# Kernel optimization log

Measured on AMD Instinct MI355X. Metric: run time of the kernel, lower is better.

The kernel has to match this reference:

```python
import jax, jax.numpy as jnp
import numpy as np

B, C, H, W = 64, 64, 56, 56
MID = 2 * C  # two output nodes concatenated
EPS = 1e-5


def _conv1x1(x, w):
    # x: [B,C,H,W], w: [O,C] (1x1 conv kernel squeezed)
    return jnp.einsum('bchw,oc->bohw', x, w)


def _bn(x, g, b, m, v):
    # eval-mode BatchNorm2d with running stats
    sc = g * jax.lax.rsqrt(v + EPS)
    return x * sc[None, :, None, None] + (b - m * sc)[None, :, None, None]


def _maxpool3(x):
    # MaxPool2d(kernel=3, stride=1, padding=1)
    return jax.lax.reduce_window(x, -jnp.inf, jax.lax.max,
                                 (1, 1, 3, 3), (1, 1, 1, 1),
                                 [(0, 0), (0, 0), (1, 1), (1, 1)])


def _avgpool3(x):
    # AvgPool2d(kernel=3, stride=1, padding=1), count_include_pad=True -> /9
    s = jax.lax.reduce_window(x, 0.0, jax.lax.add,
                              (1, 1, 3, 3), (1, 1, 1, 1),
                              [(0, 0), (0, 0), (1, 1), (1, 1)])
    return s * (1.0 / 9.0)


def setup_inputs() -> dict:
    key = jax.random.key(0)
    ks = jax.random.split(key, 11)
    x = jax.random.normal(ks[0], (B, C, H, W), dtype=jnp.float32)
    w1 = jax.random.normal(ks[1], (C, C), dtype=jnp.float32) * 0.1
    w2 = jax.random.normal(ks[2], (C, MID), dtype=jnp.float32) * 0.1
    bn1_g = 1.0 + 0.1 * jax.random.normal(ks[3], (C,), dtype=jnp.float32)
    bn1_b = 0.1 * jax.random.normal(ks[4], (C,), dtype=jnp.float32)
    bn1_m = 0.1 * jax.random.normal(ks[5], (C,), dtype=jnp.float32)
    bn1_v = jax.random.uniform(ks[6], (C,), minval=0.5, maxval=1.5, dtype=jnp.float32)
    bn2_g = 1.0 + 0.1 * jax.random.normal(ks[7], (C,), dtype=jnp.float32)
    bn2_b = 0.1 * jax.random.normal(ks[8], (C,), dtype=jnp.float32)
    bn2_m = 0.1 * jax.random.normal(ks[9], (C,), dtype=jnp.float32)
    bn2_v = jax.random.uniform(ks[10], (C,), minval=0.5, maxval=1.5, dtype=jnp.float32)
    return dict(x=x, w1=w1, w2=w2,
                bn1_g=bn1_g, bn1_b=bn1_b, bn1_m=bn1_m, bn1_v=bn1_v,
                bn2_g=bn2_g, bn2_b=bn2_b, bn2_m=bn2_m, bn2_v=bn2_v)


def reference(x, w1, w2, bn1_g, bn1_b, bn1_m, bn1_v, bn2_g, bn2_b, bn2_m, bn2_v):
    # DAG g = [[[0,1],[1,2]], [[4,3],[3]], [[5,3],[3,100]], [[4,3],[100]]]
    # topoSort order: [0, 2, 1, 3]; output nodes (ordered): [2, 3]
    node0 = jax.nn.relu(_bn(_conv1x1(x, w1), bn1_g, bn1_b, bn1_m, bn1_v))
    node1 = _maxpool3(node0)            # op type 4, pred {0}
    node2 = _avgpool3(node0)            # op type 5, pred {0}
    node3 = _maxpool3(node1) + _maxpool3(node2)  # op type 4, preds {1,2}, summed
    cat = jnp.concatenate([node2, node3], axis=1)  # [B, 2C, H, W]
    out = jax.nn.relu(_bn(_conv1x1(cat, w2), bn2_g, bn2_b, bn2_m, bn2_v))
    return out
```

## Files before the change

### kernel.cpp

```cpp
#include <hip/hip_runtime.h>
#include <cstddef>

#define EPS 1e-5f
static constexpr int Bn = 64, Cn = 64, Hn = 56, Wn = 56, HWn = Hn * Wn;
static constexpr int RB = 14;
static constexpr int NBAND = 4;
static constexpr int PR = 5;
static constexpr int SLAB5 = 2256;

typedef __attribute__((ext_vector_type(8))) short short8;
typedef __attribute__((ext_vector_type(4))) unsigned short ushort4v;
typedef __attribute__((ext_vector_type(4))) float floatx4;
typedef __attribute__((ext_vector_type(16))) float floatx16;
typedef __attribute__((ext_vector_type(4))) unsigned int uintx4;
typedef __attribute__((ext_vector_type(2))) unsigned int uintx2;

__device__ __forceinline__ unsigned pack_rne(float a, float b) {
    unsigned ua = __float_as_uint(a), ub = __float_as_uint(b);
    ua = ua + 0x7fffu + ((ua >> 16) & 1u);
    ub = ub + 0x7fffu + ((ub >> 16) & 1u);
    return __builtin_amdgcn_perm(ub, ua, 0x07060302);
}
__device__ __forceinline__ unsigned pack_trunc(float a, float b) {
    return __builtin_amdgcn_perm(__float_as_uint(b), __float_as_uint(a), 0x07060302);
}
__device__ __forceinline__ uintx2 pmax2(uintx2 a, uintx2 b) {
    ushort4v r = __builtin_elementwise_max(*(ushort4v*)&a, *(ushort4v*)&b);
    return *(uintx2*)&r;
}
__device__ __forceinline__ float bf_lo(unsigned u) { return __uint_as_float(u << 16); }
__device__ __forceinline__ float bf_hi(unsigned u) { return __uint_as_float(u & 0xffff0000u); }


__global__ __launch_bounds__(256, 3) void k1_conv1(
    const float* __restrict__ x, const float* __restrict__ w1,
    const float* __restrict__ bg, const float* __restrict__ bb,
    const float* __restrict__ bm, const float* __restrict__ bv,
    unsigned short* __restrict__ node0)
{
    __shared__ float scs[64], shs[64];
    const int tid = threadIdx.x;
    if (tid < 64) {
        float sc = bg[tid] * rsqrtf(bv[tid] + EPS);
        scs[tid] = sc;
        shs[tid] = bb[tid] - bm[tid] * sc;
    }
    __syncthreads();
    const int lane = tid & 63;
    const int wv   = tid >> 6;
    const int n    = lane & 31;
    const int h    = lane >> 5;

    short8 afr0[4], afr1[4];
    {
        const float s0 = scs[n], s1 = scs[32 + n];
        #pragma unroll
        for (int kt = 0; kt < 4; ++kt) {
            const float* wp0 = w1 + (size_t)n * 64 + kt * 16 + h * 8;
            floatx4 f0 = *(const floatx4*)wp0;
            floatx4 f1 = *(const floatx4*)(wp0 + 4);
            uintx4 u;
            u.x = pack_rne(f0[0] * s0, f0[1] * s0);
            u.y = pack_rne(f0[2] * s0, f0[3] * s0);
            u.z = pack_rne(f1[0] * s0, f1[1] * s0);
            u.w = pack_rne(f1[2] * s0, f1[3] * s0);
            afr0[kt] = *(short8*)&u;
            const float* wp1 = wp0 + 32 * 64;
            floatx4 g0 = *(const floatx4*)wp1;
            floatx4 g1 = *(const floatx4*)(wp1 + 4);
            uintx4 v;
            v.x = pack_rne(g0[0] * s1, g0[1] * s1);
            v.y = pack_rne(g0[2] * s1, g0[3] * s1);
            v.z = pack_rne(g1[0] * s1, g1[1] * s1);
            v.w = pack_rne(g1[2] * s1, g1[3] * s1);
            afr1[kt] = *(short8*)&v;
        }
    }

    const int bid = blockIdx.x;
    const int xcd = bid & 7;
    const int idx = bid >> 3;
    const int P = (xcd * 98 + idx) * 256 + wv * 64;
    const int b = P / HWn, p0 = P - b * HWn;
    const float* xb = x + (size_t)b * 64 * HWn + p0 + n;

    float f0[4][8], f1[4][8];
    #pragma unroll
    for (int kt = 0; kt < 4; ++kt)
        #pragma unroll
        for (int j = 0; j < 8; ++j) {
            const float* xp = xb + (size_t)(kt * 16 + h * 8 + j) * HWn;
            f0[kt][j] = xp[0];
            f1[kt][j] = xp[32];
        }

    #pragma unroll
    for (int s = 0; s < 2; ++s) {
        floatx16 acc0, acc1;
        #pragma unroll
        for (int i = 0; i < 16; ++i) { acc0[i] = 0.f; acc1[i] = 0.f; }

        #pragma unroll
        for (int kt = 0; kt < 4; ++kt) {
            float* fr = s ? f1[kt] : f0[kt];
            uintx4 u;
            u.x = pack_trunc(fr[0], fr[1]);
            u.y = pack_trunc(fr[2], fr[3]);
            u.z = pack_trunc(fr[4], fr[5]);
            u.w = pack_trunc(fr[6], fr[7]);
            short8 bfr = *(short8*)&u;
            acc0 = __builtin_amdgcn_mfma_f32_32x32x16_bf16(afr0[kt], bfr, acc0, 0, 0, 0);
            acc1 = __builtin_amdgcn_mfma_f32_32x32x16_bf16(afr1[kt], bfr, acc1, 0, 0, 0);
        }

        #pragma unroll
        for (int oct = 0; oct < 2; ++oct) {
            #pragma unroll
            for (int g = 0; g < 4; ++g) {
                floatx4 sh4 = *(const floatx4*)&shs[oct * 32 + g * 8 + h * 4];
                float v0 = (oct ? acc1[g * 4 + 0] : acc0[g * 4 + 0]) + sh4[0]; v0 = v0 > 0.f ? v0 : 0.f;
                float v1 = (oct ? acc1[g * 4 + 1] : acc0[g * 4 + 1]) + sh4[1]; v1 = v1 > 0.f ? v1 : 0.f;
                float v2 = (oct ? acc1[g * 4 + 2] : acc0[g * 4 + 2]) + sh4[2]; v2 = v2 > 0.f ? v2 : 0.f;
                float v3 = (oct ? acc1[g * 4 + 3] : acc0[g * 4 + 3]) + sh4[3]; v3 = v3 > 0.f ? v3 : 0.f;
                uintx2 st;
                st.x = pack_rne(v0, v1);
                st.y = pack_rne(v2, v3);
                const int chunk = oct * 4 + g;
                *(uintx2*)(node0 + ((size_t)(b * 8 + chunk) * HWn + p0 + s * 32 + n) * 8 + h * 4) = st;
            }
        }
    }
}

__global__ __launch_bounds__(1024, 1) void k23_fused(
    const unsigned short* __restrict__ node0,
    const float* __restrict__ w2,
    const float* __restrict__ bg, const float* __restrict__ bb,
    const float* __restrict__ bm, const float* __restrict__ bv,
    float* __restrict__ out)
{
    __shared__ __align__(16) unsigned short catl[2 * 16 * SLAB5 + 64];
    const int tid = threadIdx.x;
    const int lane = tid & 63;
    const int wv = tid >> 6;

    const int bid = blockIdx.x;
    const int xcd = bid & 7;
    const int jj = bid >> 3;
    const int b = xcd * 8 + (jj >> 2);
    const int band = jj & 3;
    const int lo = band * RB;

    const int chunk = wv >> 1;
    const int c0 = (wv & 1) * 28;
    const int local = lane >> 1;
    const int col = c0 - 2 + local;
    const int jh = lane & 1;
    const bool stcol = (local >= 2) & (local <= 29);
    const unsigned short* nbase = node0 + ((size_t)(b * 8 + chunk) * HWn) * 8 + jh * 4;

    const int m16 = lane & 15;
    const int q = lane >> 4;
    const int t = wv & 3;
    const int e = wv >> 2;
    short8 afr[4];
    #pragma unroll
    for (int cp = 0; cp < 4; ++cp) {
        const int c = 2 * cp + (q >> 1);
        const int chb = ((q & 1) ? 64 : 0) + 8 * c;
        const float* wp = w2 + (size_t)(t * 16 + m16) * 128 + chb;
        floatx4 f0 = *(const floatx4*)wp;
        floatx4 f1 = *(const floatx4*)(wp + 4);
        uintx4 u;
        u.x = pack_rne(f0[0], f0[1]);
        u.y = pack_rne(f0[2], f0[3]);
        u.z = pack_rne(f1[0], f1[1]);
        u.w = pack_rne(f1[2], f1[3]);
        afr[cp] = *(short8*)&u;
    }
    const int oc0 = t * 16 + q * 4;
    floatx4 g4 = *(const floatx4*)(bg + oc0);
    floatx4 bb4 = *(const floatx4*)(bb + oc0);
    floatx4 mm4 = *(const floatx4*)(bm + oc0);
    floatx4 vv4 = *(const floatx4*)(bv + oc0);
    float sc2[4], sh2[4];
    #pragma unroll
    for (int r = 0; r < 4; ++r) {
        sc2[r] = g4[r] * rsqrtf(vv4[r] + EPS);
        sh2[r] = bb4[r] - mm4[r] * sc2[r];
    }
    float* ob = out + (size_t)(b * 64 + oc0) * HWn;

    const uintx2 zz = (uintx2){0u, 0u};

    auto pool_pass = [&](int lop, int nr, unsigned short* cbuf) {
        unsigned short* cav = cbuf + (size_t)(chunk * 2) * SLAB5 + jh * 4;
        unsigned short* cmx = cav + SLAB5;
        auto loadrow = [&](int r) -> uintx2 {
            if (((unsigned)col >= (unsigned)Wn) | ((unsigned)r >= (unsigned)Hn)) return zz;
            return *(const uintx2*)(nbase + (size_t)(r * Wn + col) * 8);
        };
        float hs1[4], hs2[4];
        #pragma unroll
        for (int c = 0; c < 4; ++c) hs1[c] = hs2[c] = 0.f;
        uintx2 h5a = zz, h5b = zz, h5c = zz, h5d = zz, nh1 = zz, nh2 = zz;

        uintx2 cur = loadrow(lop - 2);
        uintx2 nxt = loadrow(lop - 1);

        for (int i = 0; i < nr + 4; ++i) {
            const int r = lop - 2 + i;
            uintx2 nx2 = (i < nr + 2) ? loadrow(r + 2) : zz;

            uintx2 D0, D1, D3, D4;
            #pragma unroll
            for (int w = 0; w < 2; ++w) {
                unsigned u = cur[w];
                D1[w] = __shfl_up(u, 2);
                D0[w] = __shfl_up(u, 4);
                D3[w] = __shfl_down(u, 2);
                D4[w] = __shfl_down(u, 4);
            }

            uintx2 hm5 = pmax2(pmax2(pmax2(D0, D1), pmax2(cur, D3)), D4);
            uintx2 m5 = pmax2(pmax2(pmax2(h5a, h5b), pmax2(h5c, h5d)), hm5);
            h5a = h5b; h5b = h5c; h5c = h5d; h5d = hm5;

            float a2[4];
            #pragma unroll
            for (int w = 0; w < 2; ++w) {
                float s0 = bf_lo(D1[w]) + bf_lo(cur[w]) + bf_lo(D3[w]);
                float s1 = bf_hi(D1[w]) + bf_hi(cur[w]) + bf_hi(D3[w]);
                a2[w * 2 + 0] = (hs2[w * 2 + 0] + hs1[w * 2 + 0] + s0) * (1.f / 9.f);
                a2[w * 2 + 1] = (hs2[w * 2 + 1] + hs1[w * 2 + 1] + s1) * (1.f / 9.f);
                hs2[w * 2 + 0] = hs1[w * 2 + 0]; hs1[w * 2 + 0] = s0;
                hs2[w * 2 + 1] = hs1[w * 2 + 1]; hs1[w * 2 + 1] = s1;
            }
            uintx2 ap;
            ap.x = pack_rne(a2[0], a2[1]);
            ap.y = pack_rne(a2[2], a2[3]);

            uintx2 al, ar;
            #pragma unroll
            for (int w = 0; w < 2; ++w) {
                al[w] = __shfl_up(ap[w], 2);
                ar[w] = __shfl_down(ap[w], 2);
            }
            uintx2 nh = pmax2(pmax2(al, ap), ar);
            uintx2 m3 = pmax2(pmax2(nh2, nh1), nh);
            nh2 = nh1; nh1 = nh;

            const int r2 = r - 1, r3 = r - 2;
            if (stcol && i >= 3 && i <= nr + 2)
                *(uintx2*)(cav + (size_t)((r2 - lop) * Wn + col) * 8) = ap;
            if (stcol && i >= 4) {
                uintx2 st;
                st.x = pack_rne(bf_lo(m5.x) + bf_lo(m3.x), bf_hi(m5.x) + bf_hi(m3.x));
                st.y = pack_rne(bf_lo(m5.y) + bf_lo(m3.y), bf_hi(m5.y) + bf_hi(m3.y));
                *(uintx2*)(cmx + (size_t)((r3 - lop) * Wn + col) * 8) = st;
            }
            cur = nxt; nxt = nx2;
        }
    };

    auto conv_pass = [&](int lop, int nr, const unsigned short* cbuf) {
        const int npxc = nr * Wn;
        const int nPT = (npxc + 15) >> 4;
        for (int k = 0; k < 5; ++k) {
            const int pt = e + 4 * k;
            if (pt >= nPT) break;
            const int px = pt * 16 + m16;
            floatx4 acc = (floatx4){0.f, 0.f, 0.f, 0.f};
            #pragma unroll
            for (int cp = 0; cp < 4; ++cp) {
                short8 bfr = *(const short8*)(cbuf + (size_t)(4 * cp + q) * SLAB5 + (size_t)px * 8);
                acc = __builtin_amdgcn_mfma_f32_16x16x32_bf16(afr[cp], bfr, acc, 0, 0, 0);
            }
            if (px < npxc) {
                #pragma unroll
                for (int r = 0; r < 4; ++r) {
                    float v = fmaf(acc[r], sc2[r], sh2[r]);
                    ob[(size_t)r * HWn + lop * Wn + px] = v > 0.f ? v : 0.f;
                }
            }
        }
    };

    unsigned short* buf0 = catl;
    unsigned short* buf1 = catl + 16 * SLAB5;

    pool_pass(lo, 5, buf0);
    __syncthreads();
    if (wv & 1) { pool_pass(lo + 5, 5, buf1); conv_pass(lo, 5, buf0); }
    else        { conv_pass(lo, 5, buf0); pool_pass(lo + 5, 5, buf1); }
    __syncthreads();
    if (wv & 1) { pool_pass(lo + 10, 4, buf0); conv_pass(lo + 5, 5, buf1); }
    else        { conv_pass(lo + 5, 5, buf1); pool_pass(lo + 10, 4, buf0); }
    __syncthreads();
    conv_pass(lo + 10, 4, buf0);
}

extern "C" void kernel_launch(void* const* d_in, const int* in_sizes, int n_in,
                              void* d_out, int out_size, void* d_ws, size_t ws_size,
                              hipStream_t stream)
{
    const float* x   = (const float*)d_in[0];
    const float* w1  = (const float*)d_in[1];
    const float* w2  = (const float*)d_in[2];
    const float* b1g = (const float*)d_in[3];
    const float* b1b = (const float*)d_in[4];
    const float* b1m = (const float*)d_in[5];
    const float* b1v = (const float*)d_in[6];
    const float* b2g = (const float*)d_in[7];
    const float* b2b = (const float*)d_in[8];
    const float* b2m = (const float*)d_in[9];
    const float* b2v = (const float*)d_in[10];

    float* out = (float*)d_out;
    unsigned short* node0 = (unsigned short*)d_ws;

    k1_conv1<<<dim3(784), dim3(256), 0, stream>>>(x, w1, b1g, b1b, b1m, b1v, node0);
    k23_fused<<<dim3(Bn * NBAND), dim3(1024), 0, stream>>>(node0, w2, b2g, b2b, b2m, b2v, out);
}
```

Measured before the change: 152.4 us.

## Shrink row bands to 8 rows with a single continuous pooling pipeline

Row bands shrink from 14 to 8 rows, giving 7 bands per image instead of 4, so the grid has more blocks. The pooling sweep no longer restarts for each 5-row sub-pass. One sliding-window state now runs across the whole band, with outputs split into two 4-row shared buffers. This removes the repeated halo row loads and recomputation between sub-passes and cuts one barrier. In exchange, more blocks recompute halo rows at band edges, and the kernel relies on the new launch grid matching the 7-band mapping, which the shown code does not confirm.

After: 156.1 us. +2.5%, slower.

```diff
diff --git a/kernel.cpp b/kernel.cpp
--- a/kernel.cpp
+++ b/kernel.cpp
@@ -3,10 +3,9 @@
 
 #define EPS 1e-5f
 static constexpr int Bn = 64, Cn = 64, Hn = 56, Wn = 56, HWn = Hn * Wn;
-static constexpr int RB = 14;
-static constexpr int NBAND = 4;
-static constexpr int PR = 5;
-static constexpr int SLAB5 = 2256;
+static constexpr int RB = 8;
+static constexpr int NBAND = 7;
+static constexpr int SLAB = 1808;
 
 typedef __attribute__((ext_vector_type(8))) short short8;
 typedef __attribute__((ext_vector_type(4))) unsigned short ushort4v;
@@ -139,7 +138,7 @@
     const float* __restrict__ bm, const float* __restrict__ bv,
     float* __restrict__ out)
 {
-    __shared__ __align__(16) unsigned short catl[2 * 16 * SLAB5 + 64];
+    __shared__ __align__(16) unsigned short catl[2 * 16 * SLAB];
     const int tid = threadIdx.x;
     const int lane = tid & 63;
     const int wv = tid >> 6;
@@ -147,8 +146,8 @@
     const int bid = blockIdx.x;
     const int xcd = bid & 7;
     const int jj = bid >> 3;
-    const int b = xcd * 8 + (jj >> 2);
-    const int band = jj & 3;
+    const int b = xcd * 8 + jj / NBAND;
+    const int band = jj % NBAND;
     const int lo = band * RB;
 
     const int chunk = wv >> 1;
@@ -158,6 +157,11 @@
     const int jh = lane & 1;
     const bool stcol = (local >= 2) & (local <= 29);
     const unsigned short* nbase = node0 + ((size_t)(b * 8 + chunk) * HWn) * 8 + jh * 4;
+
+    unsigned short* cavA = catl + (size_t)(chunk * 2) * SLAB + jh * 4;
+    unsigned short* cmxA = cavA + SLAB;
+    unsigned short* cavB = cavA + 16 * SLAB;
+    unsigned short* cmxB = cmxA + 16 * SLAB;
 
     const int m16 = lane & 15;
     const int q = lane >> 4;
@@ -192,25 +196,22 @@
     float* ob = out + (size_t)(b * 64 + oc0) * HWn;
 
     const uintx2 zz = (uintx2){0u, 0u};
-
-    auto pool_pass = [&](int lop, int nr, unsigned short* cbuf) {
-        unsigned short* cav = cbuf + (size_t)(chunk * 2) * SLAB5 + jh * 4;
-        unsigned short* cmx = cav + SLAB5;
-        auto loadrow = [&](int r) -> uintx2 {
-            if (((unsigned)col >= (unsigned)Wn) | ((unsigned)r >= (unsigned)Hn)) return zz;
-            return *(const uintx2*)(nbase + (size_t)(r * Wn + col) * 8);
-        };
-        float hs1[4], hs2[4];
-        #pragma unroll
-        for (int c = 0; c < 4; ++c) hs1[c] = hs2[c] = 0.f;
-        uintx2 h5a = zz, h5b = zz, h5c = zz, h5d = zz, nh1 = zz, nh2 = zz;
-
-        uintx2 cur = loadrow(lop - 2);
-        uintx2 nxt = loadrow(lop - 1);
-
-        for (int i = 0; i < nr + 4; ++i) {
-            const int r = lop - 2 + i;
-            uintx2 nx2 = (i < nr + 2) ? loadrow(r + 2) : zz;
+    auto loadrow = [&](int r) -> uintx2 {
+        if (((unsigned)col >= (unsigned)Wn) | ((unsigned)r >= (unsigned)Hn)) return zz;
+        return *(const uintx2*)(nbase + (size_t)(r * Wn + col) * 8);
+    };
+
+    float hs1[4], hs2[4];
+    #pragma unroll
+    for (int c = 0; c < 4; ++c) hs1[c] = hs2[c] = 0.f;
+    uintx2 h5a = zz, h5b = zz, h5c = zz, h5d = zz, nh1 = zz, nh2 = zz;
+    uintx2 cur = loadrow(lo - 2);
+    uintx2 nxt = loadrow(lo - 1);
+
+    auto pool_iters = [&](int i0, int i1) {
+        for (int i = i0; i < i1; ++i) {
+            const int r = lo - 2 + i;
+            uintx2 nx2 = (i < RB + 2) ? loadrow(r + 2) : zz;
 
             uintx2 D0, D1, D3, D4;
             #pragma unroll
@@ -251,53 +252,52 @@
             nh2 = nh1; nh1 = nh;
 
             const int r2 = r - 1, r3 = r - 2;
-            if (stcol && i >= 3 && i <= nr + 2)
-                *(uintx2*)(cav + (size_t)((r2 - lop) * Wn + col) * 8) = ap;
+            if (stcol && i >= 3 && i <= RB + 2) {
+                const int rr = r2 - lo;
+                unsigned short* cav = (rr < 4) ? cavA : cavB;
+                *(uintx2*)(cav + (size_t)((rr & 3) * Wn + col) * 8) = ap;
+            }
             if (stcol && i >= 4) {
+                const int rr = r3 - lo;
+                unsigned short* cmx = (rr < 4) ? cmxA : cmxB;
                 uintx2 st;
                 st.x = pack_rne(bf_lo(m5.x) + bf_lo(m3.x), bf_hi(m5.x) + bf_hi(m3.x));
                 st.y = pack_rne(bf_lo(m5.y) + bf_lo(m3.y), bf_hi(m5.y) + bf_hi(m3.y));
-                *(uintx2*)(cmx + (size_t)((r3 - lop) * Wn + col) * 8) = st;
+                *(uintx2*)(cmx + (size_t)((rr & 3) * Wn + col) * 8) = st;
             }
             cur = nxt; nxt = nx2;
         }
     };
 
-    auto conv_pass = [&](int lop, int nr, const unsigned short* cbuf) {
-        const int npxc = nr * Wn;
-        const int nPT = (npxc + 15) >> 4;
-        for (int k = 0; k < 5; ++k) {
+    auto conv_pass = [&](int lop, const unsigned short* cbuf) {
+        #pragma unroll
+        for (int k = 0; k < 4; ++k) {
             const int pt = e + 4 * k;
-            if (pt >= nPT) break;
+            if (pt >= 14) break;
             const int px = pt * 16 + m16;
             floatx4 acc = (floatx4){0.f, 0.f, 0.f, 0.f};
             #pragma unroll
             for (int cp = 0; cp < 4; ++cp) {
-                short8 bfr = *(const short8*)(cbuf + (size_t)(4 * cp + q) * SLAB5 + (size_t)px * 8);
+                short8 bfr = *(const short8*)(cbuf + (size_t)(4 * cp + q) * SLAB + (size_t)px * 8);
                 acc = __builtin_amdgcn_mfma_f32_16x16x32_bf16(afr[cp], bfr, acc, 0, 0, 0);
             }
-            if (px < npxc) {
-                #pragma unroll
-                for (int r = 0; r < 4; ++r) {
-                    float v = fmaf(acc[r], sc2[r], sh2[r]);
-                    ob[(size_t)r * HWn + lop * Wn + px] = v > 0.f ? v : 0.f;
-                }
+            #pragma unroll
+            for (int r = 0; r < 4; ++r) {
+                float v = fmaf(acc[r], sc2[r], sh2[r]);
+                ob[(size_t)r * HWn + lop * Wn + px] = v > 0.f ? v : 0.f;
             }
         }
     };
 
-    unsigned short* buf0 = catl;
-    unsigned short* buf1 = catl + 16 * SLAB5;
-
-    pool_pass(lo, 5, buf0);
+    const unsigned short* bufA = catl;
+    const unsigned short* bufB = catl + 16 * SLAB;
+
+    pool_iters(0, 8);
     __syncthreads();
-    if (wv & 1) { pool_pass(lo + 5, 5, buf1); conv_pass(lo, 5, buf0); }
-    else        { conv_pass(lo, 5, buf0); pool_pass(lo + 5, 5, buf1); }
+    if (wv & 1) { pool_iters(8, 12); conv_pass(lo, bufA); }
+    else        { conv_pass(lo, bufA); pool_iters(8, 12); }
     __syncthreads();
-    if (wv & 1) { pool_pass(lo + 10, 4, buf0); conv_pass(lo + 5, 5, buf1); }
-    else        { conv_pass(lo + 5, 5, buf1); pool_pass(lo + 10, 4, buf0); }
-    __syncthreads();
-    conv_pass(lo + 10, 4, buf0);
+    conv_pass(lo + 4, bufB);
 }
 
 extern "C" void kernel_launch(void* const* d_in, const int* in_sizes, int n_in,
```
